# Kernel optimization log

Hardware: AMD Instinct MI355X
Metric: run time of the kernel (lower is better)

Reference implementation:

```python
import jax, jax.numpy as jnp
import numpy as np

N = 65536      # occupied voxels
D = 96         # voxel grid extent per axis
CIN = 64
CH = 64
COUT = 16      # 8 * 2
K = 27         # 3^3 kernel offsets


def _build_neighbor_idx(rng):
    # unique occupied voxel coordinates
    lin = rng.choice(D ** 3, size=N, replace=False).astype(np.int64)
    coords = np.stack(np.unravel_index(lin, (D, D, D)), axis=1)  # [N,3]
    grid = np.full(D ** 3, -1, dtype=np.int32)
    grid[lin] = np.arange(N, dtype=np.int32)
    # 27 offsets in {-1,0,1}^3 (MinkowskiEngine kernel map, stride 1)
    offs = np.stack(np.meshgrid(*([np.arange(-1, 2)] * 3), indexing='ij'),
                    axis=-1).reshape(K, 3)
    nc = coords[:, None, :] + offs[None, :, :]            # [N,27,3]
    valid = np.all((nc >= 0) & (nc < D), axis=-1)         # [N,27]
    nlin = (nc[..., 0] * D + nc[..., 1]) * D + nc[..., 2]
    nidx = np.where(valid, grid[np.clip(nlin, 0, D ** 3 - 1)], -1)
    return nidx.astype(np.int32)                          # -1 = no neighbor


def setup_inputs() -> dict:
    key = jax.random.key(0)
    ks = jax.random.split(key, 7)
    rng = np.random.default_rng(0)
    neighbor_idx = jnp.asarray(_build_neighbor_idx(rng))
    s1 = 1.0 / np.sqrt(K * CIN)
    s2 = 1.0 / np.sqrt(K * CH)
    return {
        'x': jax.random.normal(ks[0], (N, CIN), jnp.float32),
        'neighbor_idx': neighbor_idx,
        'W1': jax.random.normal(ks[1], (K, CIN, CH), jnp.float32) * s1,
        'b1': jax.random.normal(ks[2], (CH,), jnp.float32) * 0.1,
        'W2': jax.random.normal(ks[3], (K, CH, CH), jnp.float32) * s2,
        'b2': jax.random.normal(ks[4], (CH,), jnp.float32) * 0.1,
        'W3': jax.random.normal(ks[5], (K, CH, COUT), jnp.float32) * s2,
        'b3': jax.random.normal(ks[6], (COUT,), jnp.float32) * 0.1,
    }


def _sparse_conv(feat, W, b, nidx):
    # feat: [N,Cin], W: [K,Cin,Cout], nidx: [N,K] with -1 for missing
    mask = nidx >= 0
    gathered = jnp.where(mask[..., None],
                         feat[jnp.clip(nidx, 0)], 0.0)    # [N,K,Cin]
    return jnp.einsum('nkc,kcd->nd', gathered, W) + b


def reference(x, neighbor_idx, W1, b1, W2, b2, W3, b3):
    h = jax.nn.relu(_sparse_conv(x, W1, b1, neighbor_idx))
    h = jax.nn.relu(_sparse_conv(h, W2, b2, neighbor_idx))
    return _sparse_conv(h, W3, b3, neighbor_idx)
```

## Files before the change

kernel.cpp:

```cpp
#include <hip/hip_runtime.h>
#include <hip/hip_bf16.h>
#include <stdint.h>

#define N_VOX 65536
#define NK 27
#define BR 128

typedef float f32x4 __attribute__((ext_vector_type(4)));
typedef __bf16 bf16x8 __attribute__((ext_vector_type(8)));

#define WAITVM(n) asm volatile("s_waitcnt vmcnt(" #n ")" ::: "memory")

__device__ __forceinline__ void barrier_fence() {
    asm volatile("" ::: "memory");
    __builtin_amdgcn_s_barrier();
    asm volatile("" ::: "memory");
}

__device__ __forceinline__ void gll16(const void* src, uint32_t lds_addr) {
    asm volatile("s_mov_b32 m0, %0\n\t"
                 "global_load_lds_dwordx4 %1, off"
                 :: "s"(lds_addr), "v"(src)
                 : "memory");
}

__device__ __forceinline__ void wconv_elem(const float* __restrict__ W,
                                           __bf16* __restrict__ Wt, int Dc, int i) {
    int d = i % Dc;
    int c = (i / Dc) % 64;
    int k = i / (Dc * 64);
    int off = ((d * 128 + ((c >> 3) << 4)) ^ ((d & 7) << 4)) + (c & 7) * 2;
    *(__bf16*)((char*)Wt + (size_t)k * Dc * 128 + off) = (__bf16)W[i];
}

#define PREP_CVT   2048
#define PREP_W1    432
#define PREP_W2    432
#define PREP_W3    108
#define PREP_GRID  (PREP_CVT + PREP_W1 + PREP_W2 + PREP_W3 + 1)
__global__ __launch_bounds__(256) void prep_kernel(
    const float* __restrict__ x,
    const float* __restrict__ W1, const float* __restrict__ W2, const float* __restrict__ W3,
    __bf16* __restrict__ xb, __bf16* __restrict__ Wt1, __bf16* __restrict__ Wt2,
    __bf16* __restrict__ Wt3, float* __restrict__ zp)
{
    const int b = blockIdx.x, tid = threadIdx.x;
    if (b < PREP_CVT) {
        int i = b * 256 + tid;
        const f32x4* xp = (const f32x4*)x;
        f32x4 f0 = xp[i * 2], f1 = xp[i * 2 + 1];
        bf16x8 v;
#pragma unroll
        for (int j = 0; j < 4; ++j) { v[j] = (__bf16)f0[j]; v[4 + j] = (__bf16)f1[j]; }
        ((bf16x8*)xb)[i] = v;
    } else if (b < PREP_CVT + PREP_W1) {
        wconv_elem(W1, Wt1, 64, (b - PREP_CVT) * 256 + tid);
    } else if (b < PREP_CVT + PREP_W1 + PREP_W2) {
        wconv_elem(W2, Wt2, 64, (b - PREP_CVT - PREP_W1) * 256 + tid);
    } else if (b < PREP_CVT + PREP_W1 + PREP_W2 + PREP_W3) {
        wconv_elem(W3, Wt3, 16, (b - PREP_CVT - PREP_W1 - PREP_W2) * 256 + tid);
    } else {
        if (tid < 16) ((f32x4*)zp)[tid] = (f32x4){0.f, 0.f, 0.f, 0.f};
    }
}

template <int NCOLS, bool RELU, bool OUT_F32>
__global__ __launch_bounds__(256, 2) void conv_layer(
    const __bf16* __restrict__ feat,
    const int* __restrict__ nidx,
    const __bf16* __restrict__ Wt,
    const float* __restrict__ bias,
    void* __restrict__ dst,
    const __bf16* __restrict__ zp)
{
    constexpr int MI = 2;
    constexpr int NI = NCOLS / 16;
    constexpr int ABSZ = BR * 128;
    constexpr int BSZ = NCOLS * 128;
    constexpr int BOFF = 2 * ABSZ;
    constexpr int SNOFF = BOFF + 2 * BSZ;
    __shared__ __align__(16) char lds[SNOFF + BR * NK * 4];

    const int tid = threadIdx.x;
    const int lane = tid & 63;
    const int wid = tid >> 6;
    const int col = lane & 15;
    const int kgrp = lane >> 4;
    const int row0 = blockIdx.x * BR;

    int* snid = (int*)(lds + SNOFF);
    const int* gnid = nidx + (size_t)row0 * NK;
    for (int i = tid; i < BR * NK; i += 256) {
        int r = i / NK;
        int kk = i - r * NK;
        snid[kk * BR + r] = gnid[i];
    }
    __syncthreads();

    const uint32_t ldsbase = (uint32_t)(uintptr_t)(&lds[0]);
    const int uw = __builtin_amdgcn_readfirstlane(wid);

    int rA[4], qA[4];
#pragma unroll
    for (int j = 0; j < 4; ++j) {
        int o = (wid * 4 + j) * 1024 + lane * 16;
        rA[j] = o >> 7;
        qA[j] = ((o >> 4) & 7) ^ (rA[j] & 7);
    }

    auto issue = [&](int k, int buf) {
        if constexpr (NCOLS == 64) {
#pragma unroll
            for (int j = 0; j < 2; ++j) {
                int jb = wid * 2 + j;
                const __bf16* src = Wt + (size_t)k * (NCOLS * 64) + jb * 512 + lane * 8;
                gll16(src, (uint32_t)__builtin_amdgcn_readfirstlane(
                                (int)(ldsbase + BOFF + buf * BSZ + jb * 1024)));
            }
        } else {
            if (uw < 2) {
                const __bf16* src = Wt + (size_t)k * (NCOLS * 64) + wid * 512 + lane * 8;
                gll16(src, (uint32_t)__builtin_amdgcn_readfirstlane(
                                (int)(ldsbase + BOFF + buf * BSZ + wid * 1024)));
            }
        }
#pragma unroll
        for (int j = 0; j < 4; ++j) {
            int m = snid[k * BR + rA[j]];
            const __bf16* src = (m >= 0) ? (feat + (size_t)m * 64 + qA[j] * 8) : zp;
            gll16(src, (uint32_t)__builtin_amdgcn_readfirstlane(
                            (int)(ldsbase + buf * ABSZ + (wid * 4 + j) * 1024)));
        }
    };

    f32x4 acc[MI][NI];
#pragma unroll
    for (int mi = 0; mi < MI; ++mi)
#pragma unroll
        for (int ni = 0; ni < NI; ++ni)
#pragma unroll
            for (int j = 0; j < 4; ++j) acc[mi][ni][j] = 0.f;

    issue(0, 0);

    for (int k = 0; k < NK; ++k) {
        const int cur = k & 1;
        barrier_fence();
        if (k + 1 < NK) {
            issue(k + 1, cur ^ 1);
            if constexpr (NCOLS == 64) { WAITVM(6); }
            else { if (uw < 2) { WAITVM(5); } else { WAITVM(4); } }
        } else {
            WAITVM(0);
        }
        barrier_fence();

        const char* Ac = lds + cur * ABSZ;
        const char* Bc = lds + BOFF + cur * BSZ;
        bf16x8 a[MI][2];
#pragma unroll
        for (int mi = 0; mi < MI; ++mi) {
            int ar = wid * 32 + mi * 16 + col;
#pragma unroll
            for (int kk = 0; kk < 2; ++kk)
                a[mi][kk] = *(const bf16x8*)(Ac + ((ar * 128 + kk * 64 + kgrp * 16)
                                                   ^ ((ar & 7) << 4)));
        }
#pragma unroll
        for (int kk = 0; kk < 2; ++kk)
#pragma unroll
            for (int ni = 0; ni < NI; ++ni) {
                int br = ni * 16 + col;
                bf16x8 b = *(const bf16x8*)(Bc + ((br * 128 + kk * 64 + kgrp * 16)
                                                  ^ ((br & 7) << 4)));
#pragma unroll
                for (int mi = 0; mi < MI; ++mi)
                    acc[mi][ni] = __builtin_amdgcn_mfma_f32_16x16x32_bf16(
                        a[mi][kk], b, acc[mi][ni], 0, 0, 0);
            }
    }

#pragma unroll
    for (int ni = 0; ni < NI; ++ni) {
        float bv = bias[ni * 16 + col];
#pragma unroll
        for (int mi = 0; mi < MI; ++mi) {
#pragma unroll
            for (int reg = 0; reg < 4; ++reg) {
                int r = row0 + wid * 32 + mi * 16 + kgrp * 4 + reg;
                float v = acc[mi][ni][reg] + bv;
                if (RELU) v = fmaxf(v, 0.f);
                if (OUT_F32) ((float*)dst)[(size_t)r * NCOLS + ni * 16 + col] = v;
                else ((__bf16*)dst)[(size_t)r * NCOLS + ni * 16 + col] = (__bf16)v;
            }
        }
    }
}

extern "C" void kernel_launch(void* const* d_in, const int* in_sizes, int n_in,
                              void* d_out, int out_size, void* d_ws, size_t ws_size,
                              hipStream_t stream) {
    const float* x  = (const float*)d_in[0];
    const int* nidx = (const int*)d_in[1];
    const float* W1 = (const float*)d_in[2];
    const float* b1 = (const float*)d_in[3];
    const float* W2 = (const float*)d_in[4];
    const float* b2 = (const float*)d_in[5];
    const float* W3 = (const float*)d_in[6];
    const float* b3 = (const float*)d_in[7];

    char* ws = (char*)d_ws;
    __bf16* buf0 = (__bf16*)ws;
    __bf16* buf1 = (__bf16*)(ws + 8388608);
    __bf16* Wt1  = (__bf16*)(ws + 16777216);
    __bf16* Wt2  = Wt1 + 27 * 64 * 64;
    __bf16* Wt3  = Wt2 + 27 * 64 * 64;
    __bf16* zp   = Wt3 + 27 * 16 * 64;

    prep_kernel<<<PREP_GRID, 256, 0, stream>>>(x, W1, W2, W3, buf0, Wt1, Wt2, Wt3, (float*)zp);

    dim3 grid(N_VOX / BR);
    conv_layer<64, true,  false><<<grid, 256, 0, stream>>>(buf0, nidx, Wt1, b1, buf1, zp);
    conv_layer<64, true,  false><<<grid, 256, 0, stream>>>(buf1, nidx, Wt2, b2, buf0, zp);
    conv_layer<16, false, true ><<<grid, 256, 0, stream>>>(buf0, nidx, Wt3, b3, d_out, zp);
}
```

Measured before the change: 75.59 us.

## Replace dense 27-offset gather-GEMM with compacted per-offset gather-GEMM-scatter

Adds a preprocessing pipeline (per-block histogram, single-block scan, fill) that builds per-kernel-offset lists of only the valid neighbor pairs, padded to 128-row tiles. Each layer then runs a gather-GEMM over these compacted tiles into an intermediate buffer, followed by a per-voxel reduction kernel that sums the contributions and applies bias and ReLU. This avoids gathering and multiplying zero rows for missing neighbors, which dominate at this grid sparsity. In exchange it adds several kernel launches, a round trip through the intermediate buffer for each layer, and extra bf16 rounding of partial products before the sum.

```diff
diff --git a/kernel.cpp b/kernel.cpp
--- a/kernel.cpp
+++ b/kernel.cpp
@@ -4,7 +4,6 @@
 
 #define N_VOX 65536
 #define NK 27
-#define BR 128
 
 typedef float f32x4 __attribute__((ext_vector_type(4)));
 typedef __bf16 bf16x8 __attribute__((ext_vector_type(8)));
@@ -37,13 +36,15 @@
 #define PREP_W1    432
 #define PREP_W2    432
 #define PREP_W3    108
-#define PREP_GRID  (PREP_CVT + PREP_W1 + PREP_W2 + PREP_W3 + 1)
+#define PREP_HIST  256
+#define PREP_GRID  (PREP_CVT + PREP_W1 + PREP_W2 + PREP_W3 + PREP_HIST + 1)
 __global__ __launch_bounds__(256) void prep_kernel(
-    const float* __restrict__ x,
+    const float* __restrict__ x, const int* __restrict__ nidx,
     const float* __restrict__ W1, const float* __restrict__ W2, const float* __restrict__ W3,
     __bf16* __restrict__ xb, __bf16* __restrict__ Wt1, __bf16* __restrict__ Wt2,
-    __bf16* __restrict__ Wt3, float* __restrict__ zp)
-{
+    __bf16* __restrict__ Wt3, int* __restrict__ pcnt, float* __restrict__ zp)
+{
+    __shared__ int hcnt[NK];
     const int b = blockIdx.x, tid = threadIdx.x;
     if (b < PREP_CVT) {
         int i = b * 256 + tid;
@@ -59,46 +60,118 @@
         wconv_elem(W2, Wt2, 64, (b - PREP_CVT - PREP_W1) * 256 + tid);
     } else if (b < PREP_CVT + PREP_W1 + PREP_W2 + PREP_W3) {
         wconv_elem(W3, Wt3, 16, (b - PREP_CVT - PREP_W1 - PREP_W2) * 256 + tid);
+    } else if (b < PREP_CVT + PREP_W1 + PREP_W2 + PREP_W3 + PREP_HIST) {
+        int hb = b - (PREP_CVT + PREP_W1 + PREP_W2 + PREP_W3);
+        if (tid < NK) hcnt[tid] = 0;
+        __syncthreads();
+        const int* np = nidx + ((size_t)hb * 256 + tid) * NK;
+#pragma unroll
+        for (int k = 0; k < NK; ++k)
+            if (np[k] >= 0) atomicAdd(&hcnt[k], 1);
+        __syncthreads();
+        if (tid < NK) pcnt[hb * NK + tid] = hcnt[tid];
     } else {
         if (tid < 16) ((f32x4*)zp)[tid] = (f32x4){0.f, 0.f, 0.f, 0.f};
     }
 }
 
-template <int NCOLS, bool RELU, bool OUT_F32>
-__global__ __launch_bounds__(256, 2) void conv_layer(
-    const __bf16* __restrict__ feat,
-    const int* __restrict__ nidx,
-    const __bf16* __restrict__ Wt,
-    const float* __restrict__ bias,
-    void* __restrict__ dst,
-    const __bf16* __restrict__ zp)
-{
-    constexpr int MI = 2;
+#define MAXTILES 2048
+__global__ __launch_bounds__(256) void scan_kernel(
+    const int* __restrict__ pcnt, int* __restrict__ bbase,
+    int* __restrict__ tileoff, int* __restrict__ mlist)
+{
+    __shared__ int wsum[4];
+    __shared__ int P[NK];
+    __shared__ int toff[NK + 1];
+    const int tid = threadIdx.x, lane = tid & 63, w = tid >> 6;
+    int e[NK];
+#pragma unroll
+    for (int k = 0; k < NK; ++k) {
+        int v = pcnt[tid * NK + k];
+        int s = v;
+#pragma unroll
+        for (int d = 1; d < 64; d <<= 1) {
+            int t2 = __shfl_up(s, d, 64);
+            if (lane >= d) s += t2;
+        }
+        if (lane == 63) wsum[w] = s;
+        __syncthreads();
+        int wb = 0;
+#pragma unroll
+        for (int j = 0; j < 4; ++j) if (j < w) wb += wsum[j];
+        e[k] = wb + s - v;
+        if (tid == 255) P[k] = wb + s;
+        __syncthreads();
+    }
+    if (tid == 0) {
+        int run = 0;
+        for (int k = 0; k < NK; ++k) {
+            toff[k] = run;
+            run += (P[k] + 127) >> 7;
+            if (run > MAXTILES) run = MAXTILES;
+        }
+        toff[NK] = run;
+    }
+    __syncthreads();
+    if (tid < NK + 1) tileoff[tid] = toff[tid];
+#pragma unroll
+    for (int k = 0; k < NK; ++k)
+        bbase[tid * NK + k] = toff[k] * 128 + e[k];
+    for (int k = 0; k < NK; ++k) {
+        int s0 = toff[k] * 128 + P[k];
+        int e0 = toff[k + 1] * 128;
+        for (int i = s0 + tid; i < e0; i += 256) mlist[i] = -1;
+    }
+}
+
+__global__ __launch_bounds__(256) void fill_kernel(
+    const int* __restrict__ nidx, const int* __restrict__ bbase,
+    int* __restrict__ mlist, int* __restrict__ pos)
+{
+    __shared__ int lcnt[NK];
+    __shared__ int bb[NK];
+    const int tid = threadIdx.x;
+    if (tid < NK) lcnt[tid] = 0;
+    __syncthreads();
+    const int n = blockIdx.x * 256 + tid;
+    const int* np = nidx + (size_t)n * NK;
+    int lr[NK];
+#pragma unroll
+    for (int k = 0; k < NK; ++k) {
+        int m = np[k];
+        lr[k] = (m >= 0) ? atomicAdd(&lcnt[k], 1) : -1;
+    }
+    __syncthreads();
+    if (tid < NK) bb[tid] = bbase[blockIdx.x * NK + tid];
+    __syncthreads();
+    int* pp = pos + (size_t)n * NK;
+#pragma unroll
+    for (int k = 0; k < NK; ++k) {
+        int m = np[k];
+        if (m >= 0) {
+            int s = bb[k] + lr[k];
+            mlist[s] = m;
+            pp[k] = s;
+        } else pp[k] = -1;
+    }
+}
+
+template <int NCOLS, bool YF32>
+__global__ __launch_bounds__(256, 2) void phaseA(
+    const __bf16* __restrict__ feat, const int* __restrict__ mlist,
+    const int* __restrict__ tileoff, const __bf16* __restrict__ Wt,
+    void* __restrict__ Y, const __bf16* __restrict__ zp)
+{
     constexpr int NI = NCOLS / 16;
-    constexpr int ABSZ = BR * 128;
     constexpr int BSZ = NCOLS * 128;
-    constexpr int BOFF = 2 * ABSZ;
-    constexpr int SNOFF = BOFF + 2 * BSZ;
-    __shared__ __align__(16) char lds[SNOFF + BR * NK * 4];
-
-    const int tid = threadIdx.x;
-    const int lane = tid & 63;
-    const int wid = tid >> 6;
-    const int col = lane & 15;
-    const int kgrp = lane >> 4;
-    const int row0 = blockIdx.x * BR;
-
-    int* snid = (int*)(lds + SNOFF);
-    const int* gnid = nidx + (size_t)row0 * NK;
-    for (int i = tid; i < BR * NK; i += 256) {
-        int r = i / NK;
-        int kk = i - r * NK;
-        snid[kk * BR + r] = gnid[i];
-    }
-    __syncthreads();
-
+    __shared__ __align__(16) char lds[16384 + BSZ];
+    __shared__ int stoff[NK + 1];
+    const int tid = threadIdx.x, lane = tid & 63, wid = tid >> 6;
+    const int col = lane & 15, kgrp = lane >> 4;
+    if (tid < NK + 1) stoff[tid] = tileoff[tid];
+    __syncthreads();
+    const int ntiles = stoff[NK];
     const uint32_t ldsbase = (uint32_t)(uintptr_t)(&lds[0]);
-    const int uw = __builtin_amdgcn_readfirstlane(wid);
 
     int rA[4], qA[4];
 #pragma unroll
@@ -108,92 +181,145 @@
         qA[j] = ((o >> 4) & 7) ^ (rA[j] & 7);
     }
 
-    auto issue = [&](int k, int buf) {
+    int k = 0;
+    for (int t = blockIdx.x; t < ntiles; t += gridDim.x) {
+        while (t >= stoff[k + 1]) ++k;
+        const int slot0 = t << 7;
+        __syncthreads();
         if constexpr (NCOLS == 64) {
 #pragma unroll
             for (int j = 0; j < 2; ++j) {
                 int jb = wid * 2 + j;
-                const __bf16* src = Wt + (size_t)k * (NCOLS * 64) + jb * 512 + lane * 8;
-                gll16(src, (uint32_t)__builtin_amdgcn_readfirstlane(
-                                (int)(ldsbase + BOFF + buf * BSZ + jb * 1024)));
+                gll16(Wt + (size_t)k * 4096 + jb * 512 + lane * 8,
+                      (uint32_t)__builtin_amdgcn_readfirstlane(
+                          (int)(ldsbase + 16384 + jb * 1024)));
             }
         } else {
-            if (uw < 2) {
-                const __bf16* src = Wt + (size_t)k * (NCOLS * 64) + wid * 512 + lane * 8;
-                gll16(src, (uint32_t)__builtin_amdgcn_readfirstlane(
-                                (int)(ldsbase + BOFF + buf * BSZ + wid * 1024)));
-            }
+            if (wid < 2)
+                gll16(Wt + (size_t)k * 1024 + wid * 512 + lane * 8,
+                      (uint32_t)__builtin_amdgcn_readfirstlane(
+                          (int)(ldsbase + 16384 + wid * 1024)));
         }
 #pragma unroll
         for (int j = 0; j < 4; ++j) {
-            int m = snid[k * BR + rA[j]];
+            int m = mlist[slot0 + rA[j]];
             const __bf16* src = (m >= 0) ? (feat + (size_t)m * 64 + qA[j] * 8) : zp;
             gll16(src, (uint32_t)__builtin_amdgcn_readfirstlane(
-                            (int)(ldsbase + buf * ABSZ + (wid * 4 + j) * 1024)));
-        }
-    };
-
-    f32x4 acc[MI][NI];
-#pragma unroll
-    for (int mi = 0; mi < MI; ++mi)
-#pragma unroll
-        for (int ni = 0; ni < NI; ++ni)
-#pragma unroll
-            for (int j = 0; j < 4; ++j) acc[mi][ni][j] = 0.f;
-
-    issue(0, 0);
-
-    for (int k = 0; k < NK; ++k) {
-        const int cur = k & 1;
+                           (int)(ldsbase + (wid * 4 + j) * 1024)));
+        }
+        WAITVM(0);
         barrier_fence();
-        if (k + 1 < NK) {
-            issue(k + 1, cur ^ 1);
-            if constexpr (NCOLS == 64) { WAITVM(6); }
-            else { if (uw < 2) { WAITVM(5); } else { WAITVM(4); } }
-        } else {
-            WAITVM(0);
-        }
-        barrier_fence();
-
-        const char* Ac = lds + cur * ABSZ;
-        const char* Bc = lds + BOFF + cur * BSZ;
-        bf16x8 a[MI][2];
-#pragma unroll
-        for (int mi = 0; mi < MI; ++mi) {
+
+        bf16x8 a[2][2];
+#pragma unroll
+        for (int mi = 0; mi < 2; ++mi) {
             int ar = wid * 32 + mi * 16 + col;
 #pragma unroll
             for (int kk = 0; kk < 2; ++kk)
-                a[mi][kk] = *(const bf16x8*)(Ac + ((ar * 128 + kk * 64 + kgrp * 16)
+                a[mi][kk] = *(const bf16x8*)(lds + ((ar * 128 + kk * 64 + kgrp * 16)
                                                    ^ ((ar & 7) << 4)));
         }
+        f32x4 acc[2][NI];
+#pragma unroll
+        for (int mi = 0; mi < 2; ++mi)
+#pragma unroll
+            for (int ni = 0; ni < NI; ++ni)
+#pragma unroll
+                for (int j = 0; j < 4; ++j) acc[mi][ni][j] = 0.f;
 #pragma unroll
         for (int kk = 0; kk < 2; ++kk)
 #pragma unroll
             for (int ni = 0; ni < NI; ++ni) {
                 int br = ni * 16 + col;
-                bf16x8 b = *(const bf16x8*)(Bc + ((br * 128 + kk * 64 + kgrp * 16)
-                                                  ^ ((br & 7) << 4)));
-#pragma unroll
-                for (int mi = 0; mi < MI; ++mi)
+                bf16x8 b = *(const bf16x8*)(lds + 16384 +
+                                ((br * 128 + kk * 64 + kgrp * 16) ^ ((br & 7) << 4)));
+#pragma unroll
+                for (int mi = 0; mi < 2; ++mi)
                     acc[mi][ni] = __builtin_amdgcn_mfma_f32_16x16x32_bf16(
                         a[mi][kk], b, acc[mi][ni], 0, 0, 0);
             }
-    }
-
-#pragma unroll
-    for (int ni = 0; ni < NI; ++ni) {
-        float bv = bias[ni * 16 + col];
-#pragma unroll
-        for (int mi = 0; mi < MI; ++mi) {
-#pragma unroll
-            for (int reg = 0; reg < 4; ++reg) {
-                int r = row0 + wid * 32 + mi * 16 + kgrp * 4 + reg;
-                float v = acc[mi][ni][reg] + bv;
-                if (RELU) v = fmaxf(v, 0.f);
-                if (OUT_F32) ((float*)dst)[(size_t)r * NCOLS + ni * 16 + col] = v;
-                else ((__bf16*)dst)[(size_t)r * NCOLS + ni * 16 + col] = (__bf16)v;
+#pragma unroll
+        for (int mi = 0; mi < 2; ++mi)
+#pragma unroll
+            for (int ni = 0; ni < NI; ++ni)
+#pragma unroll
+                for (int reg = 0; reg < 4; ++reg) {
+                    size_t row = slot0 + wid * 32 + mi * 16 + kgrp * 4 + reg;
+                    int c = ni * 16 + col;
+                    if constexpr (YF32)
+                        ((float*)Y)[row * 16 + c] = acc[mi][ni][reg];
+                    else
+                        ((__bf16*)Y)[row * 64 + c] = (__bf16)acc[mi][ni][reg];
+                }
+    }
+}
+
+template <bool RELU>
+__global__ __launch_bounds__(256) void phaseB64(
+    const int* __restrict__ pos, const __bf16* __restrict__ Y,
+    const float* __restrict__ bias, __bf16* __restrict__ dst)
+{
+    const int gid = blockIdx.x * 256 + threadIdx.x;
+    const int n = gid >> 2, q = gid & 3;
+    const int* pn = pos + (size_t)n * NK;
+    float acc[16];
+#pragma unroll
+    for (int i = 0; i < 16; ++i) acc[i] = bias[q * 16 + i];
+#pragma unroll
+    for (int k = 0; k < NK; ++k) {
+        int p = pn[k];
+        if (p >= 0) {
+            const bf16x8* yr = (const bf16x8*)(Y + (size_t)p * 64 + q * 16);
+            bf16x8 y0 = yr[0], y1 = yr[1];
+#pragma unroll
+            for (int i = 0; i < 8; ++i) {
+                acc[i] += (float)y0[i];
+                acc[8 + i] += (float)y1[i];
             }
         }
+    }
+    bf16x8 o0, o1;
+#pragma unroll
+    for (int i = 0; i < 8; ++i) {
+        float v0 = acc[i], v1 = acc[8 + i];
+        if (RELU) { v0 = fmaxf(v0, 0.f); v1 = fmaxf(v1, 0.f); }
+        o0[i] = (__bf16)v0;
+        o1[i] = (__bf16)v1;
+    }
+    bf16x8* dp = (bf16x8*)(dst + (size_t)n * 64 + q * 16);
+    dp[0] = o0;
+    dp[1] = o1;
+}
+
+__global__ __launch_bounds__(256) void phaseB16(
+    const int* __restrict__ pos, const float* __restrict__ Y,
+    const float* __restrict__ bias, float* __restrict__ out)
+{
+    const int n = blockIdx.x * 256 + threadIdx.x;
+    const int* pn = pos + (size_t)n * NK;
+    float acc[16];
+#pragma unroll
+    for (int i = 0; i < 16; ++i) acc[i] = bias[i];
+#pragma unroll
+    for (int k = 0; k < NK; ++k) {
+        int p = pn[k];
+        if (p >= 0) {
+            const f32x4* yr = (const f32x4*)(Y + (size_t)p * 16);
+#pragma unroll
+            for (int j = 0; j < 4; ++j) {
+                f32x4 v = yr[j];
+#pragma unroll
+                for (int i = 0; i < 4; ++i) acc[j * 4 + i] += v[i];
+            }
+        }
+    }
+    f32x4* op = (f32x4*)(out + (size_t)n * 16);
+#pragma unroll
+    for (int j = 0; j < 4; ++j) {
+        f32x4 v;
+#pragma unroll
+        for (int i = 0; i < 4; ++i) v[i] = acc[j * 4 + i];
+        op[j] = v;
     }
 }
 
@@ -211,16 +337,27 @@
 
     char* ws = (char*)d_ws;
     __bf16* buf0 = (__bf16*)ws;
-    __bf16* buf1 = (__bf16*)(ws + 8388608);
-    __bf16* Wt1  = (__bf16*)(ws + 16777216);
-    __bf16* Wt2  = Wt1 + 27 * 64 * 64;
-    __bf16* Wt3  = Wt2 + 27 * 64 * 64;
-    __bf16* zp   = Wt3 + 27 * 16 * 64;
-
-    prep_kernel<<<PREP_GRID, 256, 0, stream>>>(x, W1, W2, W3, buf0, Wt1, Wt2, Wt3, (float*)zp);
-
-    dim3 grid(N_VOX / BR);
-    conv_layer<64, true,  false><<<grid, 256, 0, stream>>>(buf0, nidx, Wt1, b1, buf1, zp);
-    conv_layer<64, true,  false><<<grid, 256, 0, stream>>>(buf1, nidx, Wt2, b2, buf0, zp);
-    conv_layer<16, false, true ><<<grid, 256, 0, stream>>>(buf0, nidx, Wt3, b3, d_out, zp);
-}
+    __bf16* buf1 = (__bf16*)(ws + (8u << 20));
+    __bf16* Wt1  = (__bf16*)(ws + (16u << 20));
+    __bf16* Wt2  = (__bf16*)(ws + (16u << 20) + 262144);
+    __bf16* Wt3  = (__bf16*)(ws + (16u << 20) + 524288);
+    __bf16* zp   = (__bf16*)(ws + (16u << 20) + 786432);
+    int* pcnt    = (int*)(ws + (16u << 20) + 851968);
+    int* bbase   = (int*)(ws + (16u << 20) + 917504);
+    int* tileoff = (int*)(ws + (16u << 20) + 983040);
+    int* pos     = (int*)(ws + (17u << 20));
+    int* mlist   = (int*)(ws + (24u << 20));
+    void* Ybuf   = (void*)(ws + (25u << 20));
+
+    prep_kernel<<<PREP_GRID, 256, 0, stream>>>(x, nidx, W1, W2, W3,
+                                               buf0, Wt1, Wt2, Wt3, pcnt, (float*)zp);
+    scan_kernel<<<1, 256, 0, stream>>>(pcnt, bbase, tileoff, mlist);
+    fill_kernel<<<256, 256, 0, stream>>>(nidx, bbase, mlist, pos);
+
+    phaseA<64, false><<<2048, 256, 0, stream>>>(buf0, mlist, tileoff, Wt1, Ybuf, zp);
+    phaseB64<true><<<N_VOX * 4 / 256, 256, 0, stream>>>(pos, (const __bf16*)Ybuf, b1, buf1);
+    phaseA<64, false><<<2048, 256, 0, stream>>>(buf1, mlist, tileoff, Wt2, Ybuf, zp);
+    phaseB64<true><<<N_VOX * 4 / 256, 256, 0, stream>>>(pos, (const __bf16*)Ybuf, b2, buf0);
+    phaseA<16, true><<<2048, 256, 0, stream>>>(buf0, mlist, tileoff, Wt3, Ybuf, zp);
+    phaseB16<<<N_VOX / 256, 256, 0, stream>>>(pos, (const float*)Ybuf, b3, (float*)d_out);
+}
```

Result: slower. 139.0 us (+83.9%).

## Halve row tile to 64, split warps over rows and columns, raise occupancy

Applied to the files above, without the earlier changes.

Block row tile drops from 128 to 64, so the grid doubles to 1024 blocks, and launch bounds allow 4 blocks per CU instead of 2. For 64-column layers the four waves split 2x2 over rows and columns; for the 16-column layer they split over rows only. The neighbor-index LDS table gets a new permuted layout, so each lane can fetch two gather indices with one 8-byte read. The aim is more waves in flight to hide the latency of the random gathers, at the cost of fetching the weight slice for each k twice as often per output row.

```diff
diff --git a/kernel.cpp b/kernel.cpp
--- a/kernel.cpp
+++ b/kernel.cpp
@@ -4,9 +4,10 @@
 
 #define N_VOX 65536
 #define NK 27
-#define BR 128
+#define BR 64
 
 typedef float f32x4 __attribute__((ext_vector_type(4)));
+typedef int   i32x2 __attribute__((ext_vector_type(2)));
 typedef __bf16 bf16x8 __attribute__((ext_vector_type(8)));
 
 #define WAITVM(n) asm volatile("s_waitcnt vmcnt(" #n ")" ::: "memory")
@@ -65,7 +66,7 @@
 }
 
 template <int NCOLS, bool RELU, bool OUT_F32>
-__global__ __launch_bounds__(256, 2) void conv_layer(
+__global__ __launch_bounds__(256, 4) void conv_layer(
     const __bf16* __restrict__ feat,
     const int* __restrict__ nidx,
     const __bf16* __restrict__ Wt,
@@ -73,8 +74,10 @@
     void* __restrict__ dst,
     const __bf16* __restrict__ zp)
 {
-    constexpr int MI = 2;
-    constexpr int NI = NCOLS / 16;
+    constexpr int WC = (NCOLS == 64) ? 2 : 1;
+    constexpr int WR = 4 / WC;
+    constexpr int MI = BR / (WR * 16);
+    constexpr int NI = NCOLS / (WC * 16);
     constexpr int ABSZ = BR * 128;
     constexpr int BSZ = NCOLS * 128;
     constexpr int BOFF = 2 * ABSZ;
@@ -84,6 +87,8 @@
     const int tid = threadIdx.x;
     const int lane = tid & 63;
     const int wid = tid >> 6;
+    const int wr = wid / WC;
+    const int wc = wid % WC;
     const int col = lane & 15;
     const int kgrp = lane >> 4;
     const int row0 = blockIdx.x * BR;
@@ -93,43 +98,39 @@
     for (int i = tid; i < BR * NK; i += 256) {
         int r = i / NK;
         int kk = i - r * NK;
-        snid[kk * BR + r] = gnid[i];
+        snid[kk * 64 + (r & 7) * 8 + (r >> 3)] = gnid[i];
     }
     __syncthreads();
 
     const uint32_t ldsbase = (uint32_t)(uintptr_t)(&lds[0]);
-    const int uw = __builtin_amdgcn_readfirstlane(wid);
-
-    int rA[4], qA[4];
-#pragma unroll
-    for (int j = 0; j < 4; ++j) {
-        int o = (wid * 4 + j) * 1024 + lane * 16;
-        rA[j] = o >> 7;
-        qA[j] = ((o >> 4) & 7) ^ (rA[j] & 7);
-    }
-
-    auto issue = [&](int k, int buf) {
+    const int qA = ((lane & 7) ^ (lane >> 3)) << 4;
+
+    auto issueB = [&](int k, int buf) {
         if constexpr (NCOLS == 64) {
 #pragma unroll
             for (int j = 0; j < 2; ++j) {
                 int jb = wid * 2 + j;
-                const __bf16* src = Wt + (size_t)k * (NCOLS * 64) + jb * 512 + lane * 8;
-                gll16(src, (uint32_t)__builtin_amdgcn_readfirstlane(
-                                (int)(ldsbase + BOFF + buf * BSZ + jb * 1024)));
+                gll16(Wt + (size_t)k * 4096 + jb * 512 + lane * 8,
+                      (uint32_t)__builtin_amdgcn_readfirstlane(
+                          (int)(ldsbase + BOFF + buf * BSZ + jb * 1024)));
             }
         } else {
-            if (uw < 2) {
-                const __bf16* src = Wt + (size_t)k * (NCOLS * 64) + wid * 512 + lane * 8;
-                gll16(src, (uint32_t)__builtin_amdgcn_readfirstlane(
-                                (int)(ldsbase + BOFF + buf * BSZ + wid * 1024)));
-            }
-        }
-#pragma unroll
-        for (int j = 0; j < 4; ++j) {
-            int m = snid[k * BR + rA[j]];
-            const __bf16* src = (m >= 0) ? (feat + (size_t)m * 64 + qA[j] * 8) : zp;
+            if (wid < 2)
+                gll16(Wt + (size_t)k * 1024 + wid * 512 + lane * 8,
+                      (uint32_t)__builtin_amdgcn_readfirstlane(
+                          (int)(ldsbase + BOFF + buf * BSZ + wid * 1024)));
+        }
+    };
+
+    auto issueA = [&](int k, int buf) {
+        i32x2 mv = *(const i32x2*)(snid + k * 64 + (lane >> 3) * 8 + wid * 2);
+#pragma unroll
+        for (int j = 0; j < 2; ++j) {
+            int m = mv[j];
+            const __bf16* src = (m >= 0)
+                ? (const __bf16*)((const char*)feat + (size_t)m * 128 + qA) : zp;
             gll16(src, (uint32_t)__builtin_amdgcn_readfirstlane(
-                            (int)(ldsbase + buf * ABSZ + (wid * 4 + j) * 1024)));
+                           (int)(ldsbase + buf * ABSZ + (wid * 2 + j) * 1024)));
         }
     };
 
@@ -141,57 +142,67 @@
 #pragma unroll
             for (int j = 0; j < 4; ++j) acc[mi][ni][j] = 0.f;
 
-    issue(0, 0);
-
-    for (int k = 0; k < NK; ++k) {
-        const int cur = k & 1;
-        barrier_fence();
-        if (k + 1 < NK) {
-            issue(k + 1, cur ^ 1);
-            if constexpr (NCOLS == 64) { WAITVM(6); }
-            else { if (uw < 2) { WAITVM(5); } else { WAITVM(4); } }
-        } else {
-            WAITVM(0);
-        }
-        barrier_fence();
-
-        const char* Ac = lds + cur * ABSZ;
-        const char* Bc = lds + BOFF + cur * BSZ;
-        bf16x8 a[MI][2];
+    auto compute = [&](int k) {
+        const char* Ac = lds + (k & 1) * ABSZ;
+        const char* Bc = lds + BOFF + (k & 1) * BSZ;
+        bf16x8 a[MI][2], b[NI][2];
 #pragma unroll
         for (int mi = 0; mi < MI; ++mi) {
-            int ar = wid * 32 + mi * 16 + col;
+            int ar = wr * (MI * 16) + mi * 16 + col;
 #pragma unroll
             for (int kk = 0; kk < 2; ++kk)
                 a[mi][kk] = *(const bf16x8*)(Ac + ((ar * 128 + kk * 64 + kgrp * 16)
                                                    ^ ((ar & 7) << 4)));
         }
 #pragma unroll
+        for (int ni = 0; ni < NI; ++ni) {
+            int br = wc * (NI * 16) + ni * 16 + col;
+#pragma unroll
+            for (int kk = 0; kk < 2; ++kk)
+                b[ni][kk] = *(const bf16x8*)(Bc + ((br * 128 + kk * 64 + kgrp * 16)
+                                                   ^ ((br & 7) << 4)));
+        }
+#pragma unroll
         for (int kk = 0; kk < 2; ++kk)
 #pragma unroll
-            for (int ni = 0; ni < NI; ++ni) {
-                int br = ni * 16 + col;
-                bf16x8 b = *(const bf16x8*)(Bc + ((br * 128 + kk * 64 + kgrp * 16)
-                                                  ^ ((br & 7) << 4)));
-#pragma unroll
-                for (int mi = 0; mi < MI; ++mi)
+            for (int mi = 0; mi < MI; ++mi)
+#pragma unroll
+                for (int ni = 0; ni < NI; ++ni)
                     acc[mi][ni] = __builtin_amdgcn_mfma_f32_16x16x32_bf16(
-                        a[mi][kk], b, acc[mi][ni], 0, 0, 0);
-            }
+                        a[mi][kk], b[ni][kk], acc[mi][ni], 0, 0, 0);
+    };
+
+    issueB(0, 0);
+    issueA(0, 0);
+
+    for (int k = 0; k < NK; ++k) {
+        const int buf = k & 1;
+        barrier_fence();
+        if (k + 1 < NK) {
+            issueB(k + 1, buf ^ 1);
+            issueA(k + 1, buf ^ 1);
+            if constexpr (NCOLS == 64) { WAITVM(4); }
+            else { if (wid < 2) { WAITVM(3); } else { WAITVM(2); } }
+        } else {
+            WAITVM(0);
+        }
+        barrier_fence();
+        compute(k);
     }
 
 #pragma unroll
     for (int ni = 0; ni < NI; ++ni) {
-        float bv = bias[ni * 16 + col];
+        int c = wc * (NI * 16) + ni * 16 + col;
+        float bv = bias[c];
 #pragma unroll
         for (int mi = 0; mi < MI; ++mi) {
 #pragma unroll
             for (int reg = 0; reg < 4; ++reg) {
-                int r = row0 + wid * 32 + mi * 16 + kgrp * 4 + reg;
+                int r = row0 + wr * (MI * 16) + mi * 16 + kgrp * 4 + reg;
                 float v = acc[mi][ni][reg] + bv;
                 if (RELU) v = fmaxf(v, 0.f);
-                if (OUT_F32) ((float*)dst)[(size_t)r * NCOLS + ni * 16 + col] = v;
-                else ((__bf16*)dst)[(size_t)r * NCOLS + ni * 16 + col] = (__bf16)v;
+                if (OUT_F32) ((float*)dst)[(size_t)r * NCOLS + c] = v;
+                else ((__bf16*)dst)[(size_t)r * NCOLS + c] = (__bf16)v;
             }
         }
     }
```

Result: faster. 68.96 us, median of 2 (-8.8%).
